# Optimization experiments

Measured on AMD Instinct MI355X. Metric: run time of the kernel, lower is better.

Reference implementation:

```python
import jax, jax.numpy as jnp
import numpy as np

B, S, U, H = 4, 2048, 1024, 8
HD = U // H
EPS = 1e-8


def setup_inputs() -> dict:
    key = jax.random.key(0)
    ks = jax.random.split(key, 10)
    sc = 1.0 / np.sqrt(U)
    x = jax.random.normal(ks[0], (B, S, U), dtype=jnp.float32)
    Wq = jax.random.normal(ks[1], (U, U), dtype=jnp.float32) * sc
    bq = jnp.zeros((U,), dtype=jnp.float32)
    Wk = jax.random.normal(ks[2], (U, U), dtype=jnp.float32) * sc
    bk = jnp.zeros((U,), dtype=jnp.float32)
    Wv = jax.random.normal(ks[3], (U, U), dtype=jnp.float32) * sc
    bv = jnp.zeros((U,), dtype=jnp.float32)
    Wr = jax.random.normal(ks[4], (U, U), dtype=jnp.float32) * sc
    br = jnp.zeros((U,), dtype=jnp.float32)
    gamma = jnp.ones((U,), dtype=jnp.float32)
    beta = jnp.zeros((U,), dtype=jnp.float32)
    return {"x": x, "Wq": Wq, "bq": bq, "Wk": Wk, "bk": bk, "Wv": Wv,
            "bv": bv, "Wr": Wr, "br": br, "gamma": gamma, "beta": beta}


def reference(x, Wq, bq, Wk, bk, Wv, bv, Wr, br, gamma, beta):
    relu = jax.nn.relu
    q = relu(jnp.einsum('bsu,uv->bsv', x, Wq) + bq)
    k = relu(jnp.einsum('bsu,uv->bsv', x, Wk) + bk)
    v = relu(jnp.einsum('bsu,uv->bsv', x, Wv) + bv)
    res = relu(jnp.einsum('bsu,uv->bsv', x, Wr) + br)
    # Faithful to the original: a raw reshape (NOT split+transpose head split).
    q = q.reshape(B * H, S, HD)
    k = k.reshape(B * H, S, HD)
    v = v.reshape(B * H, S, HD)
    scores = jnp.einsum('nqd,nkd->nqk', q, k) / jnp.sqrt(jnp.float32(HD))
    weights = jax.nn.softmax(scores, axis=-1)
    # dropout_rate = 0.0 -> identity
    attn = jnp.einsum('nqk,nkd->nqd', weights, v)
    attn = attn.reshape(B, S, U)
    out = relu(attn + res)
    # custom LayerNorm (biased variance, eps inside sqrt)
    mean = jnp.mean(out, axis=-1, keepdims=True)
    var = jnp.mean(jnp.square(out - mean), axis=-1, keepdims=True)
    normed = (out - mean) / jnp.sqrt(var + EPS)
    return gamma * normed + beta
```

## Files before the change

kernel.cpp:

```cpp
#include <hip/hip_runtime.h>

typedef _Float16 half8_t __attribute__((ext_vector_type(8)));
typedef _Float16 half4_t __attribute__((ext_vector_type(4)));
typedef float floatx4 __attribute__((ext_vector_type(4)));

#define S_LEN 2048
#define U_DIM 1024
#define HD 128
#define M_TOT 8192
#define NHEADS 32

__device__ __forceinline__ void stage16(void* lds_base, const void* g_lane, int lane) {
#if defined(__has_builtin) && __has_builtin(__builtin_amdgcn_global_load_lds)
    __builtin_amdgcn_global_load_lds(
        (const __attribute__((address_space(1))) unsigned int*)g_lane,
        (__attribute__((address_space(3))) unsigned int*)lds_base, 16, 0, 0);
#else
    *(float4*)((char*)lds_base + lane * 16) = *(const float4*)g_lane;
#endif
}

__global__ __launch_bounds__(256) void k_convert_x(const float* __restrict__ x,
                                                   _Float16* __restrict__ xh) {
    size_t i = (size_t)blockIdx.x * 256 + threadIdx.x;
    float4 v = ((const float4*)x)[i];
    half4_t h;
    h[0] = (_Float16)v.x; h[1] = (_Float16)v.y;
    h[2] = (_Float16)v.z; h[3] = (_Float16)v.w;
    ((half4_t*)xh)[i] = h;
}

__global__ __launch_bounds__(256) void k_transpose_w(const float* __restrict__ Wq,
                                                     const float* __restrict__ Wk,
                                                     const float* __restrict__ Wv,
                                                     const float* __restrict__ Wr,
                                                     _Float16* __restrict__ wt) {
    const int z = blockIdx.z;
    const float* W = (z == 0) ? Wq : (z == 1) ? Wk : (z == 2) ? Wv : Wr;
    _Float16* o = wt + (size_t)z * U_DIM * U_DIM;
    __shared__ float t[64][65];
    const int n0 = blockIdx.x * 64, k0 = blockIdx.y * 64;
    const int tid = threadIdx.x;
    for (int c = tid; c < 1024; c += 256) {
        int kk = c >> 4, nn = (c & 15) * 4;
        float4 v = *(const float4*)&W[(size_t)(k0 + kk) * U_DIM + n0 + nn];
        t[kk][nn] = v.x; t[kk][nn + 1] = v.y; t[kk][nn + 2] = v.z; t[kk][nn + 3] = v.w;
    }
    __syncthreads();
    for (int c = tid; c < 512; c += 256) {
        int nn = c >> 3, ks = (c & 7) * 8;
        half8_t h;
        for (int i = 0; i < 8; i++) h[i] = (_Float16)t[ks + i][nn];
        *(half8_t*)&o[(size_t)(n0 + nn) * U_DIM + k0 + ks] = h;
    }
}

__global__ __launch_bounds__(256) void k_qkvr_gemm(const _Float16* __restrict__ xh,
                                                   const _Float16* __restrict__ wt,
                                                   const float* __restrict__ bq,
                                                   const float* __restrict__ bk,
                                                   const float* __restrict__ bv,
                                                   const float* __restrict__ br,
                                                   _Float16* __restrict__ qh,
                                                   _Float16* __restrict__ kh,
                                                   _Float16* __restrict__ vh,
                                                   _Float16* __restrict__ resh) {
    const int z = blockIdx.z;
    const int m0 = blockIdx.x * 128;
    const int n0 = blockIdx.y * 128;
    const _Float16* wz = wt + (size_t)z * U_DIM * U_DIM;

    __shared__ __align__(16) _Float16 As[128][32];
    __shared__ __align__(16) _Float16 Bs[128][32];
    __shared__ __align__(16) _Float16 Cs[128][136];

    const int tid = threadIdx.x;
    const int wave = tid >> 6, lane = tid & 63;
    const int lrow = lane & 15, quad = lane >> 4;
    const int wm = (wave >> 1) * 64, wn = (wave & 1) * 64;

    floatx4 acc[4][4];
    for (int i = 0; i < 4; i++)
        for (int j = 0; j < 4; j++) acc[i][j] = (floatx4)0.0f;

    const char* xb = (const char*)xh;
    const char* wb = (const char*)wz;
    const int lr4 = lane >> 2, lc4 = (lane & 3) * 16;

    for (int k0 = 0; k0 < U_DIM; k0 += 32) {
        for (int t = 0; t < 2; t++) {
            int c = wave * 2 + t;
            stage16((char*)As + c * 1024,
                    xb + (size_t)(m0 + c * 16 + lr4) * 2048 + k0 * 2 + lc4, lane);
            stage16((char*)Bs + c * 1024,
                    wb + (size_t)(n0 + c * 16 + lr4) * 2048 + k0 * 2 + lc4, lane);
        }
        __syncthreads();
        half8_t af[4], bf[4];
        for (int i = 0; i < 4; i++) af[i] = *(const half8_t*)&As[wm + i * 16 + lrow][quad * 8];
        for (int j = 0; j < 4; j++) bf[j] = *(const half8_t*)&Bs[wn + j * 16 + lrow][quad * 8];
        for (int i = 0; i < 4; i++)
            for (int j = 0; j < 4; j++)
                acc[i][j] = __builtin_amdgcn_mfma_f32_16x16x32_f16(af[i], bf[j], acc[i][j], 0, 0, 0);
        __syncthreads();
    }

    const float* bias = (z == 0) ? bq : (z == 1) ? bk : (z == 2) ? bv : br;
    _Float16* dst = (z == 0) ? qh : (z == 1) ? kh : (z == 2) ? vh : resh;

    for (int i = 0; i < 4; i++) {
        for (int j = 0; j < 4; j++) {
            int col = wn + j * 16 + lrow;
            float bcol = bias[n0 + col];
            for (int r = 0; r < 4; r++) {
                float v = acc[i][j][r] + bcol;
                Cs[wm + i * 16 + quad * 4 + r][col] = (_Float16)(v > 0.f ? v : 0.f);
            }
        }
    }
    __syncthreads();
    for (int c = tid; c < 2048; c += 256) {
        int row = c >> 4, seg = (c & 15) * 8;
        *(half8_t*)&dst[(size_t)(m0 + row) * U_DIM + n0 + seg] = *(half8_t*)&Cs[row][seg];
    }
}

__global__ __launch_bounds__(256) void k_transpose_v(const _Float16* __restrict__ vh,
                                                     _Float16* __restrict__ vt) {
    const int n = blockIdx.z;
    const int s0 = blockIdx.x * 64, d0 = blockIdx.y * 64;
    const _Float16* V = vh + (size_t)n * S_LEN * HD;
    _Float16* O = vt + (size_t)n * HD * S_LEN;
    __shared__ _Float16 t[64][72];
    const int tid = threadIdx.x;
    for (int c = tid; c < 512; c += 256) {
        int srow = c >> 3, off = (c & 7) * 8;
        *(half8_t*)&t[srow][off] = *(const half8_t*)&V[(size_t)(s0 + srow) * HD + d0 + off];
    }
    __syncthreads();
    for (int c = tid; c < 512; c += 256) {
        int drow = c >> 3, soff = (c & 7) * 8;
        half8_t h;
        for (int i = 0; i < 8; i++) h[i] = t[soff + i][drow];
        *(half8_t*)&O[(size_t)(d0 + drow) * S_LEN + s0 + soff] = h;
    }
}

__global__ __launch_bounds__(256, 2) void k_flash(const _Float16* __restrict__ qh,
                                                  const _Float16* __restrict__ kh,
                                                  const _Float16* __restrict__ vt,
                                                  _Float16* __restrict__ attnh) {
    const int head = blockIdx.x + 8 * (blockIdx.y & 3);
    const int m0 = (int)(blockIdx.y >> 2) * 128;
    const _Float16* Q = qh + (size_t)head * S_LEN * HD;
    const _Float16* K = kh + (size_t)head * S_LEN * HD;
    const _Float16* Vt = vt + (size_t)head * HD * S_LEN;

    __shared__ __align__(16) char smem[50176];
    _Float16* Ks = (_Float16*)smem;
    _Float16* Vs = (_Float16*)(smem + 16384);
    _Float16* Ps = (_Float16*)(smem + 32768);

    const int tid = threadIdx.x;
    const int w = tid >> 6, lane = tid & 63;
    const int lrow = lane & 15, quad = lane >> 4;
    const int lr4 = lane >> 2, lc4 = (lane & 3) * 16;

    half8_t qf[2][4];
    for (int i = 0; i < 2; i++)
        for (int k0 = 0; k0 < 4; k0++)
            qf[i][k0] = *(const half8_t*)&Q[(size_t)(m0 + w * 32 + i * 16 + lrow) * HD + k0 * 32 + quad * 8];

    floatx4 acc_o[2][8];
    for (int i = 0; i < 2; i++)
        for (int j = 0; j < 8; j++) acc_o[i][j] = (floatx4)0.0f;
    float lp[2][4];
    for (int i = 0; i < 2; i++)
        for (int r = 0; r < 4; r++) lp[i][r] = 0.0f;

    const float C1 = 0.12751742f;
    const char* Kb = (const char*)K;
    const char* Vb = (const char*)Vt;

    for (int kt = 0; kt < 32; ++kt) {
        if (kt) __syncthreads();
        for (int t = 0; t < 4; t++) {
            stage16(smem + (w * 4 + t) * 1024,
                    Kb + (size_t)(kt * 64 + t * 16 + lr4) * 256 + w * 64 + lc4, lane);
        }
        for (int t = 0; t < 4; t++) {
            int c = w * 4 + t;
            int k0s = c >> 3, dg = c & 7;
            stage16(smem + 16384 + c * 1024,
                    Vb + (size_t)(dg * 16 + lr4) * (S_LEN * 2) + (size_t)(kt * 64 + k0s * 32) * 2 + lc4,
                    lane);
        }
        __syncthreads();

        floatx4 acc_s[2][4];
        for (int i = 0; i < 2; i++)
            for (int j = 0; j < 4; j++) acc_s[i][j] = (floatx4)0.0f;
        for (int k0 = 0; k0 < 4; k0++) {
            half8_t bf[4];
            for (int j = 0; j < 4; j++)
                bf[j] = *(const half8_t*)&Ks[k0 * 2048 + (j * 16 + lrow) * 32 + quad * 8];
            for (int i = 0; i < 2; i++)
                for (int j = 0; j < 4; j++)
                    acc_s[i][j] = __builtin_amdgcn_mfma_f32_16x16x32_f16(qf[i][k0], bf[j], acc_s[i][j], 0, 0, 0);
        }

        for (int i = 0; i < 2; i++)
            for (int j = 0; j < 4; j++)
                for (int r = 0; r < 4; r++) {
                    float p = exp2f(fmaf(acc_s[i][j][r], C1, -6.0f));
                    lp[i][r] += p;
                    Ps[(w * 32 + i * 16 + quad * 4 + r) * 68 + j * 16 + lrow] = (_Float16)p;
                }

        for (int k0s = 0; k0s < 2; k0s++) {
            half8_t af[2];
            for (int i = 0; i < 2; i++)
                af[i] = *(const half8_t*)&Ps[(w * 32 + i * 16 + lrow) * 68 + k0s * 32 + quad * 8];
            for (int j = 0; j < 8; j++) {
                half8_t bv = *(const half8_t*)&Vs[k0s * 4096 + (j * 16 + lrow) * 32 + quad * 8];
                for (int i = 0; i < 2; i++)
                    acc_o[i][j] = __builtin_amdgcn_mfma_f32_16x16x32_f16(af[i], bv, acc_o[i][j], 0, 0, 0);
            }
        }
    }

    float inv[2][4];
    for (int i = 0; i < 2; i++)
        for (int r = 0; r < 4; r++) {
            float l = lp[i][r];
            l += __shfl_xor(l, 1, 64);
            l += __shfl_xor(l, 2, 64);
            l += __shfl_xor(l, 4, 64);
            l += __shfl_xor(l, 8, 64);
            inv[i][r] = 1.0f / l;
        }

    __syncthreads();
    _Float16* Os = (_Float16*)smem;
    for (int i = 0; i < 2; i++)
        for (int j = 0; j < 8; j++)
            for (int r = 0; r < 4; r++)
                Os[(w * 32 + i * 16 + quad * 4 + r) * 136 + j * 16 + lrow] =
                    (_Float16)(acc_o[i][j][r] * inv[i][r]);
    __syncthreads();
    const size_t base = (size_t)head * S_LEN * HD;
    for (int c = tid; c < 2048; c += 256) {
        int row = c >> 4, seg = (c & 15) * 8;
        *(half8_t*)&attnh[base + (size_t)(m0 + row) * HD + seg] = *(half8_t*)&Os[row * 136 + seg];
    }
}

__global__ __launch_bounds__(256) void k_ln(const _Float16* __restrict__ attnh,
                                            const _Float16* __restrict__ resh,
                                            const float* __restrict__ gamma,
                                            const float* __restrict__ beta,
                                            float* __restrict__ out) {
    const size_t row = blockIdx.x;
    const int tid = threadIdx.x;
    half4_t av = ((const half4_t*)(attnh + row * U_DIM))[tid];
    half4_t rv = ((const half4_t*)(resh + row * U_DIM))[tid];
    float o[4];
    float s1 = 0.f, s2 = 0.f;
    for (int i = 0; i < 4; i++) {
        o[i] = fmaxf((float)av[i] + (float)rv[i], 0.f);
        s1 += o[i];
        s2 += o[i] * o[i];
    }
    for (int off = 32; off; off >>= 1) {
        s1 += __shfl_xor(s1, off, 64);
        s2 += __shfl_xor(s2, off, 64);
    }
    __shared__ float red[8];
    const int wv = tid >> 6;
    if ((tid & 63) == 0) { red[wv] = s1; red[4 + wv] = s2; }
    __syncthreads();
    float ts1 = red[0] + red[1] + red[2] + red[3];
    float ts2 = red[4] + red[5] + red[6] + red[7];
    float mean = ts1 * (1.0f / 1024.0f);
    float var = ts2 * (1.0f / 1024.0f) - mean * mean;
    float rstd = rsqrtf(var + 1e-8f);
    float4 gv = ((const float4*)gamma)[tid];
    float4 bv = ((const float4*)beta)[tid];
    float4 ov;
    ov.x = gv.x * (o[0] - mean) * rstd + bv.x;
    ov.y = gv.y * (o[1] - mean) * rstd + bv.y;
    ov.z = gv.z * (o[2] - mean) * rstd + bv.z;
    ov.w = gv.w * (o[3] - mean) * rstd + bv.w;
    ((float4*)(out + row * U_DIM))[tid] = ov;
}

extern "C" void kernel_launch(void* const* d_in, const int* in_sizes, int n_in,
                              void* d_out, int out_size, void* d_ws, size_t ws_size,
                              hipStream_t stream) {
    const float* x     = (const float*)d_in[0];
    const float* Wq    = (const float*)d_in[1];
    const float* bq    = (const float*)d_in[2];
    const float* Wk    = (const float*)d_in[3];
    const float* bk    = (const float*)d_in[4];
    const float* Wv    = (const float*)d_in[5];
    const float* bv    = (const float*)d_in[6];
    const float* Wr    = (const float*)d_in[7];
    const float* br    = (const float*)d_in[8];
    const float* gamma = (const float*)d_in[9];
    const float* beta  = (const float*)d_in[10];
    float* out = (float*)d_out;

    char* p = (char*)d_ws;
    _Float16* xh = (_Float16*)p;    p += (size_t)M_TOT * U_DIM * 2;
    _Float16* wt = (_Float16*)p;    p += (size_t)4 * U_DIM * U_DIM * 2;
    _Float16* qh = (_Float16*)p;    p += (size_t)M_TOT * U_DIM * 2;
    _Float16* kh = (_Float16*)p;    p += (size_t)M_TOT * U_DIM * 2;
    _Float16* vh = (_Float16*)p;    p += (size_t)M_TOT * U_DIM * 2;
    _Float16* vt = (_Float16*)p;    p += (size_t)M_TOT * U_DIM * 2;
    _Float16* resh  = (_Float16*)p; p += (size_t)M_TOT * U_DIM * 2;
    _Float16* attnh = (_Float16*)p;

    k_convert_x<<<8192, 256, 0, stream>>>(x, xh);
    k_transpose_w<<<dim3(16, 16, 4), 256, 0, stream>>>(Wq, Wk, Wv, Wr, wt);
    k_qkvr_gemm<<<dim3(64, 8, 4), 256, 0, stream>>>(xh, wt, bq, bk, bv, br, qh, kh, vh, resh);
    k_transpose_v<<<dim3(32, 2, 32), 256, 0, stream>>>(vh, vt);
    k_flash<<<dim3(8, 64), 256, 0, stream>>>(qh, kh, vt, attnh);
    k_ln<<<8192, 256, 0, stream>>>(attnh, resh, gamma, beta, out);
}
```

Baseline: 329.9 us.

## Split flash attention across eight waves with transposed score MFMA

```diff
diff --git a/kernel.cpp b/kernel.cpp
--- a/kernel.cpp
+++ b/kernel.cpp
@@ -146,17 +146,17 @@
     }
 }
 
-__global__ __launch_bounds__(256, 2) void k_flash(const _Float16* __restrict__ qh,
+__global__ __launch_bounds__(512, 4) void k_flash(const _Float16* __restrict__ qh,
                                                   const _Float16* __restrict__ kh,
                                                   const _Float16* __restrict__ vt,
                                                   _Float16* __restrict__ attnh) {
     const int head = blockIdx.x + 8 * (blockIdx.y & 3);
     const int m0 = (int)(blockIdx.y >> 2) * 128;
     const _Float16* Q = qh + (size_t)head * S_LEN * HD;
-    const _Float16* K = kh + (size_t)head * S_LEN * HD;
-    const _Float16* Vt = vt + (size_t)head * HD * S_LEN;
-
-    __shared__ __align__(16) char smem[50176];
+    const char* Kb = (const char*)(kh + (size_t)head * S_LEN * HD);
+    const char* Vb = (const char*)(vt + (size_t)head * HD * S_LEN);
+
+    __shared__ __align__(16) char smem[51200];
     _Float16* Ks = (_Float16*)smem;
     _Float16* Vs = (_Float16*)(smem + 16384);
     _Float16* Ps = (_Float16*)(smem + 32768);
@@ -166,90 +166,76 @@
     const int lrow = lane & 15, quad = lane >> 4;
     const int lr4 = lane >> 2, lc4 = (lane & 3) * 16;
 
-    half8_t qf[2][4];
-    for (int i = 0; i < 2; i++)
-        for (int k0 = 0; k0 < 4; k0++)
-            qf[i][k0] = *(const half8_t*)&Q[(size_t)(m0 + w * 32 + i * 16 + lrow) * HD + k0 * 32 + quad * 8];
-
-    floatx4 acc_o[2][8];
-    for (int i = 0; i < 2; i++)
-        for (int j = 0; j < 8; j++) acc_o[i][j] = (floatx4)0.0f;
-    float lp[2][4];
-    for (int i = 0; i < 2; i++)
-        for (int r = 0; r < 4; r++) lp[i][r] = 0.0f;
+    half8_t qf[4];
+    for (int k0 = 0; k0 < 4; k0++)
+        qf[k0] = *(const half8_t*)&Q[(size_t)(m0 + w * 16 + lrow) * HD + k0 * 32 + quad * 8];
+
+    floatx4 acc_o[8];
+    for (int j = 0; j < 8; j++) acc_o[j] = (floatx4)0.0f;
+    float lp = 0.0f;
 
     const float C1 = 0.12751742f;
-    const char* Kb = (const char*)K;
-    const char* Vb = (const char*)Vt;
 
     for (int kt = 0; kt < 32; ++kt) {
         if (kt) __syncthreads();
-        for (int t = 0; t < 4; t++) {
-            stage16(smem + (w * 4 + t) * 1024,
-                    Kb + (size_t)(kt * 64 + t * 16 + lr4) * 256 + w * 64 + lc4, lane);
-        }
-        for (int t = 0; t < 4; t++) {
-            int c = w * 4 + t;
-            int k0s = c >> 3, dg = c & 7;
-            stage16(smem + 16384 + c * 1024,
-                    Vb + (size_t)(dg * 16 + lr4) * (S_LEN * 2) + (size_t)(kt * 64 + k0s * 32) * 2 + lc4,
-                    lane);
+        if (w < 4) {
+            for (int t = 0; t < 4; t++)
+                stage16(smem + (w * 4 + t) * 1024,
+                        Kb + (size_t)(kt * 64 + t * 16 + lr4) * 256 + w * 64 + lc4, lane);
+        } else {
+            for (int t = 0; t < 4; t++) {
+                int c = (w - 4) * 4 + t;
+                int k0s = c >> 3, dg = c & 7;
+                stage16(smem + 16384 + c * 1024,
+                        Vb + (size_t)(dg * 16 + lr4) * 4096 + kt * 128 + k0s * 64 + lc4, lane);
+            }
         }
         __syncthreads();
 
-        floatx4 acc_s[2][4];
-        for (int i = 0; i < 2; i++)
-            for (int j = 0; j < 4; j++) acc_s[i][j] = (floatx4)0.0f;
-        for (int k0 = 0; k0 < 4; k0++) {
-            half8_t bf[4];
-            for (int j = 0; j < 4; j++)
-                bf[j] = *(const half8_t*)&Ks[k0 * 2048 + (j * 16 + lrow) * 32 + quad * 8];
-            for (int i = 0; i < 2; i++)
-                for (int j = 0; j < 4; j++)
-                    acc_s[i][j] = __builtin_amdgcn_mfma_f32_16x16x32_f16(qf[i][k0], bf[j], acc_s[i][j], 0, 0, 0);
-        }
-
-        for (int i = 0; i < 2; i++)
-            for (int j = 0; j < 4; j++)
-                for (int r = 0; r < 4; r++) {
-                    float p = exp2f(fmaf(acc_s[i][j][r], C1, -6.0f));
-                    lp[i][r] += p;
-                    Ps[(w * 32 + i * 16 + quad * 4 + r) * 68 + j * 16 + lrow] = (_Float16)p;
-                }
+        floatx4 acc_t[4];
+        for (int j = 0; j < 4; j++) acc_t[j] = (floatx4)0.0f;
+        for (int k0 = 0; k0 < 4; k0++)
+            for (int j = 0; j < 4; j++) {
+                half8_t kf = *(const half8_t*)&Ks[(k0 * 4 + j) * 512 + lrow * 32 + quad * 8];
+                acc_t[j] = __builtin_amdgcn_mfma_f32_16x16x32_f16(kf, qf[k0], acc_t[j], 0, 0, 0);
+            }
+
+        for (int j = 0; j < 4; j++) {
+            half4_t ph;
+            for (int r = 0; r < 4; r++) {
+                float p = exp2f(fmaf(acc_t[j][r], C1, -6.0f));
+                lp += p;
+                ph[r] = (_Float16)p;
+            }
+            *(half4_t*)&Ps[(w * 16 + lrow) * 72 + j * 16 + quad * 4] = ph;
+        }
 
         for (int k0s = 0; k0s < 2; k0s++) {
-            half8_t af[2];
-            for (int i = 0; i < 2; i++)
-                af[i] = *(const half8_t*)&Ps[(w * 32 + i * 16 + lrow) * 68 + k0s * 32 + quad * 8];
+            half4_t a0 = *(const half4_t*)&Ps[(w * 16 + lrow) * 72 + k0s * 32 + quad * 8];
+            half4_t a1 = *(const half4_t*)&Ps[(w * 16 + lrow) * 72 + k0s * 32 + quad * 8 + 4];
+            half8_t af = __builtin_shufflevector(a0, a1, 0, 1, 2, 3, 4, 5, 6, 7);
             for (int j = 0; j < 8; j++) {
-                half8_t bv = *(const half8_t*)&Vs[k0s * 4096 + (j * 16 + lrow) * 32 + quad * 8];
-                for (int i = 0; i < 2; i++)
-                    acc_o[i][j] = __builtin_amdgcn_mfma_f32_16x16x32_f16(af[i], bv, acc_o[i][j], 0, 0, 0);
-            }
-        }
-    }
-
-    float inv[2][4];
-    for (int i = 0; i < 2; i++)
-        for (int r = 0; r < 4; r++) {
-            float l = lp[i][r];
-            l += __shfl_xor(l, 1, 64);
-            l += __shfl_xor(l, 2, 64);
-            l += __shfl_xor(l, 4, 64);
-            l += __shfl_xor(l, 8, 64);
-            inv[i][r] = 1.0f / l;
-        }
+                half8_t bv = *(const half8_t*)&Vs[(k0s * 8 + j) * 512 + lrow * 32 + quad * 8];
+                acc_o[j] = __builtin_amdgcn_mfma_f32_16x16x32_f16(af, bv, acc_o[j], 0, 0, 0);
+            }
+        }
+    }
+
+    lp += __shfl_xor(lp, 16, 64);
+    lp += __shfl_xor(lp, 32, 64);
+    float inv[4];
+    for (int r = 0; r < 4; r++)
+        inv[r] = 1.0f / __shfl(lp, quad * 4 + r, 64);
 
     __syncthreads();
     _Float16* Os = (_Float16*)smem;
-    for (int i = 0; i < 2; i++)
-        for (int j = 0; j < 8; j++)
-            for (int r = 0; r < 4; r++)
-                Os[(w * 32 + i * 16 + quad * 4 + r) * 136 + j * 16 + lrow] =
-                    (_Float16)(acc_o[i][j][r] * inv[i][r]);
+    for (int j = 0; j < 8; j++)
+        for (int r = 0; r < 4; r++)
+            Os[(w * 16 + quad * 4 + r) * 136 + j * 16 + lrow] =
+                (_Float16)(acc_o[j][r] * inv[r]);
     __syncthreads();
     const size_t base = (size_t)head * S_LEN * HD;
-    for (int c = tid; c < 2048; c += 256) {
+    for (int c = tid; c < 2048; c += 512) {
         int row = c >> 4, seg = (c & 15) * 8;
         *(half8_t*)&attnh[base + (size_t)(m0 + row) * HD + seg] = *(half8_t*)&Os[row * 136 + seg];
     }
@@ -324,6 +310,6 @@
     k_transpose_w<<<dim3(16, 16, 4), 256, 0, stream>>>(Wq, Wk, Wv, Wr, wt);
     k_qkvr_gemm<<<dim3(64, 8, 4), 256, 0, stream>>>(xh, wt, bq, bk, bv, br, qh, kh, vh, resh);
     k_transpose_v<<<dim3(32, 2, 32), 256, 0, stream>>>(vh, vt);
-    k_flash<<<dim3(8, 64), 256, 0, stream>>>(qh, kh, vt, attnh);
+    k_flash<<<dim3(8, 64), 512, 0, stream>>>(qh, kh, vt, attnh);
     k_ln<<<8192, 256, 0, stream>>>(attnh, resh, gamma, beta, out);
 }
```

After: 313.4 us. -5.0%, faster.

## Stage LDS tiles in MFMA fragment order and compute transposed scores

Applied to the files above, without the earlier changes.

```diff
diff --git a/kernel.cpp b/kernel.cpp
--- a/kernel.cpp
+++ b/kernel.cpp
@@ -70,8 +70,8 @@
     const int n0 = blockIdx.y * 128;
     const _Float16* wz = wt + (size_t)z * U_DIM * U_DIM;
 
-    __shared__ __align__(16) _Float16 As[128][32];
-    __shared__ __align__(16) _Float16 Bs[128][32];
+    __shared__ __align__(16) char AsB[8192];
+    __shared__ __align__(16) char BsB[8192];
     __shared__ __align__(16) _Float16 Cs[128][136];
 
     const int tid = threadIdx.x;
@@ -85,20 +85,21 @@
 
     const char* xb = (const char*)xh;
     const char* wb = (const char*)wz;
-    const int lr4 = lane >> 2, lc4 = (lane & 3) * 16;
 
     for (int k0 = 0; k0 < U_DIM; k0 += 32) {
         for (int t = 0; t < 2; t++) {
             int c = wave * 2 + t;
-            stage16((char*)As + c * 1024,
-                    xb + (size_t)(m0 + c * 16 + lr4) * 2048 + k0 * 2 + lc4, lane);
-            stage16((char*)Bs + c * 1024,
-                    wb + (size_t)(n0 + c * 16 + lr4) * 2048 + k0 * 2 + lc4, lane);
+            stage16(AsB + c * 1024,
+                    xb + (size_t)(m0 + c * 16 + lrow) * 2048 + k0 * 2 + quad * 16, lane);
+            stage16(BsB + c * 1024,
+                    wb + (size_t)(n0 + c * 16 + lrow) * 2048 + k0 * 2 + quad * 16, lane);
         }
         __syncthreads();
         half8_t af[4], bf[4];
-        for (int i = 0; i < 4; i++) af[i] = *(const half8_t*)&As[wm + i * 16 + lrow][quad * 8];
-        for (int j = 0; j < 4; j++) bf[j] = *(const half8_t*)&Bs[wn + j * 16 + lrow][quad * 8];
+        for (int i = 0; i < 4; i++)
+            af[i] = *(const half8_t*)(AsB + ((wave >> 1) * 4 + i) * 1024 + lane * 16);
+        for (int j = 0; j < 4; j++)
+            bf[j] = *(const half8_t*)(BsB + ((wave & 1) * 4 + j) * 1024 + lane * 16);
         for (int i = 0; i < 4; i++)
             for (int j = 0; j < 4; j++)
                 acc[i][j] = __builtin_amdgcn_mfma_f32_16x16x32_f16(af[i], bf[j], acc[i][j], 0, 0, 0);
@@ -153,18 +154,15 @@
     const int head = blockIdx.x + 8 * (blockIdx.y & 3);
     const int m0 = (int)(blockIdx.y >> 2) * 128;
     const _Float16* Q = qh + (size_t)head * S_LEN * HD;
-    const _Float16* K = kh + (size_t)head * S_LEN * HD;
-    const _Float16* Vt = vt + (size_t)head * HD * S_LEN;
-
-    __shared__ __align__(16) char smem[50176];
-    _Float16* Ks = (_Float16*)smem;
-    _Float16* Vs = (_Float16*)(smem + 16384);
+    const char* Kb = (const char*)(kh + (size_t)head * S_LEN * HD);
+    const char* Vb = (const char*)(vt + (size_t)head * HD * S_LEN);
+
+    __shared__ __align__(16) char smem[51200];
     _Float16* Ps = (_Float16*)(smem + 32768);
 
     const int tid = threadIdx.x;
     const int w = tid >> 6, lane = tid & 63;
     const int lrow = lane & 15, quad = lane >> 4;
-    const int lr4 = lane >> 2, lc4 = (lane & 3) * 16;
 
     half8_t qf[2][4];
     for (int i = 0; i < 2; i++)
@@ -174,55 +172,53 @@
     floatx4 acc_o[2][8];
     for (int i = 0; i < 2; i++)
         for (int j = 0; j < 8; j++) acc_o[i][j] = (floatx4)0.0f;
-    float lp[2][4];
-    for (int i = 0; i < 2; i++)
-        for (int r = 0; r < 4; r++) lp[i][r] = 0.0f;
+    float lp[2] = {0.0f, 0.0f};
 
     const float C1 = 0.12751742f;
-    const char* Kb = (const char*)K;
-    const char* Vb = (const char*)Vt;
 
     for (int kt = 0; kt < 32; ++kt) {
         if (kt) __syncthreads();
         for (int t = 0; t < 4; t++) {
-            stage16(smem + (w * 4 + t) * 1024,
-                    Kb + (size_t)(kt * 64 + t * 16 + lr4) * 256 + w * 64 + lc4, lane);
+            int c = w * 4 + t;
+            int k0 = c >> 2, j = c & 3;
+            stage16(smem + c * 1024,
+                    Kb + (size_t)(kt * 64 + j * 16 + lrow) * 256 + k0 * 64 + quad * 16, lane);
         }
         for (int t = 0; t < 4; t++) {
             int c = w * 4 + t;
             int k0s = c >> 3, dg = c & 7;
             stage16(smem + 16384 + c * 1024,
-                    Vb + (size_t)(dg * 16 + lr4) * (S_LEN * 2) + (size_t)(kt * 64 + k0s * 32) * 2 + lc4,
-                    lane);
+                    Vb + (size_t)(dg * 16 + lrow) * 4096 + kt * 128 + k0s * 64 + quad * 16, lane);
         }
         __syncthreads();
 
-        floatx4 acc_s[2][4];
+        floatx4 acc_t[2][4];
         for (int i = 0; i < 2; i++)
-            for (int j = 0; j < 4; j++) acc_s[i][j] = (floatx4)0.0f;
-        for (int k0 = 0; k0 < 4; k0++) {
-            half8_t bf[4];
-            for (int j = 0; j < 4; j++)
-                bf[j] = *(const half8_t*)&Ks[k0 * 2048 + (j * 16 + lrow) * 32 + quad * 8];
-            for (int i = 0; i < 2; i++)
-                for (int j = 0; j < 4; j++)
-                    acc_s[i][j] = __builtin_amdgcn_mfma_f32_16x16x32_f16(qf[i][k0], bf[j], acc_s[i][j], 0, 0, 0);
-        }
+            for (int j = 0; j < 4; j++) acc_t[i][j] = (floatx4)0.0f;
+        for (int k0 = 0; k0 < 4; k0++)
+            for (int j = 0; j < 4; j++) {
+                half8_t kf = *(const half8_t*)(smem + (k0 * 4 + j) * 1024 + lane * 16);
+                for (int i = 0; i < 2; i++)
+                    acc_t[i][j] = __builtin_amdgcn_mfma_f32_16x16x32_f16(kf, qf[i][k0], acc_t[i][j], 0, 0, 0);
+            }
 
         for (int i = 0; i < 2; i++)
-            for (int j = 0; j < 4; j++)
+            for (int j = 0; j < 4; j++) {
+                half4_t ph;
                 for (int r = 0; r < 4; r++) {
-                    float p = exp2f(fmaf(acc_s[i][j][r], C1, -6.0f));
-                    lp[i][r] += p;
-                    Ps[(w * 32 + i * 16 + quad * 4 + r) * 68 + j * 16 + lrow] = (_Float16)p;
+                    float p = exp2f(fmaf(acc_t[i][j][r], C1, -6.0f));
+                    lp[i] += p;
+                    ph[r] = (_Float16)p;
                 }
+                *(half4_t*)&Ps[(w * 32 + i * 16 + lrow) * 72 + j * 16 + quad * 4] = ph;
+            }
 
         for (int k0s = 0; k0s < 2; k0s++) {
             half8_t af[2];
             for (int i = 0; i < 2; i++)
-                af[i] = *(const half8_t*)&Ps[(w * 32 + i * 16 + lrow) * 68 + k0s * 32 + quad * 8];
+                af[i] = *(const half8_t*)&Ps[(w * 32 + i * 16 + lrow) * 72 + k0s * 32 + quad * 8];
             for (int j = 0; j < 8; j++) {
-                half8_t bv = *(const half8_t*)&Vs[k0s * 4096 + (j * 16 + lrow) * 32 + quad * 8];
+                half8_t bv = *(const half8_t*)(smem + 16384 + (k0s * 8 + j) * 1024 + lane * 16);
                 for (int i = 0; i < 2; i++)
                     acc_o[i][j] = __builtin_amdgcn_mfma_f32_16x16x32_f16(af[i], bv, acc_o[i][j], 0, 0, 0);
             }
@@ -230,15 +226,12 @@
     }
 
     float inv[2][4];
-    for (int i = 0; i < 2; i++)
-        for (int r = 0; r < 4; r++) {
-            float l = lp[i][r];
-            l += __shfl_xor(l, 1, 64);
-            l += __shfl_xor(l, 2, 64);
-            l += __shfl_xor(l, 4, 64);
-            l += __shfl_xor(l, 8, 64);
-            inv[i][r] = 1.0f / l;
-        }
+    for (int i = 0; i < 2; i++) {
+        lp[i] += __shfl_xor(lp[i], 16, 64);
+        lp[i] += __shfl_xor(lp[i], 32, 64);
+        for (int r = 0; r < 4; r++)
+            inv[i][r] = 1.0f / __shfl(lp[i], quad * 4 + r, 64);
+    }
 
     __syncthreads();
     _Float16* Os = (_Float16*)smem;
```

New measurement: 355.2 us. 7.7% more time.
